# Performance work log

Hardware: AMD Instinct MI355X
Metric: run time of the kernel (lower is better)

## Reference

```python
import jax, jax.numpy as jnp
import numpy as np

B, T, H, W, C = 2, 8, 32, 32, 192
DI, N, K, DTR = 384, 16, 4, 12   # d_inner=2*dim, d_state, scan directions, dt_rank=ceil(dim/16)
LT, HID = 77, 768
L = T * H * W


def setup_inputs() -> dict:
    key = jax.random.key(0)
    ks = jax.random.split(key, 16)
    r = lambda i, shape, s=1.0: jax.random.normal(ks[i], shape, dtype=jnp.float32) * s
    return {
        "x": r(0, (B, T, H, W, C)),
        "text": r(1, (B, LT, C)),
        "cpe1_w": r(2, (C, 1, 3, 3, 3), 0.05), "cpe1_b": jnp.zeros((C,), jnp.float32),
        "cpe2_w": r(3, (C, 1, 3, 3, 3), 0.05), "cpe2_b": jnp.zeros((C,), jnp.float32),
        "norm1_g": jnp.ones((C,), jnp.float32), "norm1_b": jnp.zeros((C,), jnp.float32),
        "norm2_g": jnp.ones((C,), jnp.float32), "norm2_b": jnp.zeros((C,), jnp.float32),
        "in_proj_w": r(4, (2 * DI, C), 0.02), "in_proj_b": jnp.zeros((2 * DI,), jnp.float32),
        "text_proj_w": r(5, (DI, C), 0.02), "text_proj_b": jnp.zeros((DI,), jnp.float32),
        "conv_w": r(6, (DI, 1, 3, 3, 3), 0.05), "conv_b": jnp.zeros((DI,), jnp.float32),
        "x_proj_w": r(7, (K, DTR + 2 * N, DI), 0.02),
        "dt_proj_w": r(8, (K, DI, DTR), 0.1), "dt_proj_b": r(9, (K, DI), 0.1),
        "A_log": jnp.log(jnp.tile(jnp.arange(1.0, N + 1.0, dtype=jnp.float32)[None, None, :], (K, DI, 1))),
        "Ds": jnp.ones((K, DI), jnp.float32),
        "out_norm_g": jnp.ones((DI,), jnp.float32), "out_norm_b": jnp.zeros((DI,), jnp.float32),
        "out_proj_w": r(10, (C, DI), 0.02),
        "fc1_w": r(11, (HID, C), 0.02), "fc1_b": jnp.zeros((HID,), jnp.float32),
        "fc2_w": r(12, (C, HID), 0.02), "fc2_b": jnp.zeros((C,), jnp.float32),
    }


def _ln(x, g, b, eps=1e-6):
    m = x.mean(-1, keepdims=True)
    v = jnp.mean((x - m) ** 2, -1, keepdims=True)
    return (x - m) * jax.lax.rsqrt(v + eps) * g + b


def _dwconv3d(x, w, b):  # x [B, Ch, T, H, W], depthwise 3x3x3, SAME padding
    y = jax.lax.conv_general_dilated(x, w, (1, 1, 1), 'SAME',
                                     feature_group_count=x.shape[1],
                                     dimension_numbers=('NCDHW', 'OIDHW', 'NCDHW'))
    return y + b[None, :, None, None, None]


def _cpe(x, w, b):  # conv positional encoding, channels-last in/out
    return jnp.transpose(_dwconv3d(jnp.transpose(x, (0, 4, 1, 2, 3)), w, b), (0, 2, 3, 4, 1))


def _ss2d(x, text, p):
    # in-projection -> (x, z) gate split
    xz = x @ p['in_proj_w'].T + p['in_proj_b']           # [B,T,H,W,2*DI]
    xi, z = jnp.split(xz, 2, axis=-1)
    # text conditioning (pooled text tokens -> channel bias)
    cond = jax.nn.silu(text.mean(1) @ p['text_proj_w'].T + p['text_proj_b'])  # [B,DI]
    xi = xi + cond[:, None, None, None, :]
    # depthwise conv3d + SiLU
    xc = jax.nn.silu(_dwconv3d(jnp.transpose(xi, (0, 4, 1, 2, 3)), p['conv_w'], p['conv_b']))  # [B,DI,T,H,W]
    # cross-scan: (t,h,w), (t,w,h) and their reversals
    x0 = xc.reshape(B, DI, L)
    x1 = jnp.swapaxes(xc, 3, 4).reshape(B, DI, L)
    xs = jnp.stack([x0, x1, jnp.flip(x0, -1), jnp.flip(x1, -1)], 1)  # [B,K,DI,L]
    # per-direction projections
    xdbl = jnp.einsum('bkdl,kcd->bkcl', xs, p['x_proj_w'])
    dtr, Bm, Cm = jnp.split(xdbl, [DTR, DTR + N], axis=2)            # [B,K,DTR,L],[B,K,N,L],[B,K,N,L]
    dt = jax.nn.softplus(jnp.einsum('bkrl,kdr->bkdl', dtr, p['dt_proj_w']) + p['dt_proj_b'][None, :, :, None])
    A = -jnp.exp(p['A_log'])                                          # [K,DI,N]
    def step(h, inp):
        u_l, dt_l, B_l, C_l = inp
        h = h * jnp.exp(dt_l[..., None] * A) + (dt_l * u_l)[..., None] * B_l[:, :, None, :]
        return h, jnp.einsum('bkdn,bkn->bkd', h, C_l)
    seq = (xs.transpose(3, 0, 1, 2), dt.transpose(3, 0, 1, 2),
           Bm.transpose(3, 0, 1, 2), Cm.transpose(3, 0, 1, 2))
    _, ys = jax.lax.scan(step, jnp.zeros((B, K, DI, N), xs.dtype), seq)  # ys [L,B,K,DI]
    ys = ys.transpose(1, 2, 3, 0) + p['Ds'][None, :, :, None] * xs       # [B,K,DI,L]
    # merge the 4 directions back into (t,h,w) order
    unt = lambda y: jnp.swapaxes(y.reshape(B, DI, T, W, H), 3, 4).reshape(B, DI, L)
    y = ys[:, 0] + jnp.flip(ys[:, 2], -1) + unt(ys[:, 1]) + unt(jnp.flip(ys[:, 3], -1))
    y = _ln(y.transpose(0, 2, 1), p['out_norm_g'], p['out_norm_b']).reshape(B, T, H, W, DI)
    y = y * jax.nn.silu(z)
    return y @ p['out_proj_w'].T


def reference(x, text, cpe1_w, cpe1_b, cpe2_w, cpe2_b, norm1_g, norm1_b, norm2_g, norm2_b,
              in_proj_w, in_proj_b, text_proj_w, text_proj_b, conv_w, conv_b,
              x_proj_w, dt_proj_w, dt_proj_b, A_log, Ds, out_norm_g, out_norm_b, out_proj_w,
              fc1_w, fc1_b, fc2_w, fc2_b):
    p = dict(in_proj_w=in_proj_w, in_proj_b=in_proj_b, text_proj_w=text_proj_w,
             text_proj_b=text_proj_b, conv_w=conv_w, conv_b=conv_b, x_proj_w=x_proj_w,
             dt_proj_w=dt_proj_w, dt_proj_b=dt_proj_b, A_log=A_log, Ds=Ds,
             out_norm_g=out_norm_g, out_norm_b=out_norm_b, out_proj_w=out_proj_w)
    x = x + _cpe(x, cpe1_w, cpe1_b)
    x = x + _ss2d(_ln(x, norm1_g, norm1_b), text, p)
    x = x + _cpe(x, cpe2_w, cpe2_b)
    h = _ln(x, norm2_g, norm2_b)
    x = x + (jax.nn.gelu(h @ fc1_w.T + fc1_b) @ fc2_w.T + fc2_b)
    return x
```

## Files before the change

### kernel.cpp

```cpp
#include <hip/hip_runtime.h>
#include <hip/hip_bf16.h>

#define DEV __device__ __forceinline__

namespace {

constexpr int cB = 2, cT = 8, cH = 32, cW = 32, cC = 192;
constexpr int cDI = 384, cN = 16, cK = 4, cDTR = 12, cLT = 77, cHID = 768;
constexpr int cL  = cT * cH * cW;
constexpr int cBL = cB * cL;
constexpr int SEG = 128, SEGLEN = cL / SEG;
constexpr int XROW = cDTR + 2 * cN;
constexpr int XSTR = 48;

typedef __attribute__((ext_vector_type(8))) short bf16x8;
typedef __attribute__((ext_vector_type(4))) float f32x4;
typedef __attribute__((ext_vector_type(4))) short short4v;

DEV float bfu2f(unsigned short u) { return __uint_as_float(((unsigned)u) << 16); }
DEV float ldsel(const void* p, size_t i, int f32) {
  return f32 ? ((const float*)p)[i] : bfu2f(((const unsigned short*)p)[i]);
}
template <int F32>
DEV float4 ld4(const void* p, size_t e) {
  if (F32) return *(const float4*)((const float*)p + e);
  ushort4 u = *(const ushort4*)((const unsigned short*)p + e);
  return make_float4(bfu2f(u.x), bfu2f(u.y), bfu2f(u.z), bfu2f(u.w));
}
DEV short f2bf(float f) {
  unsigned u = __float_as_uint(f);
  u += 0x7fffu + ((u >> 16) & 1u);
  return (short)(u >> 16);
}
DEV float siluf(float x) { return x / (1.f + __expf(-x)); }
DEV float softplusf(float x) { return (x > 20.f) ? x : __logf(1.f + __expf(x)); }
DEV float gelut(float x) {
  float u = 0.7978845608028654f * (x + 0.044715f * x * x * x);
  float e = __expf(2.f * u);
  float th = 1.f - 2.f / (e + 1.f);
  return 0.5f * x * (1.f + th);
}

template <int BS>
DEV void blkreduce2(float& a, float& b) {
  __shared__ float ra[BS], rb[BS];
  int t = threadIdx.x;
  ra[t] = a; rb[t] = b; __syncthreads();
#pragma unroll
  for (int s = BS / 2; s > 0; s >>= 1) {
    if (t < s) { ra[t] += ra[t + s]; rb[t] += rb[t + s]; }
    __syncthreads();
  }
  a = ra[0]; b = rb[0];
  __syncthreads();
}

__global__ void __launch_bounds__(256) detect_kernel(
    const unsigned short* __restrict__ xa, const unsigned short* __restrict__ wp,
    int* __restrict__ flg) {
  __shared__ int cnt[2];
  if (threadIdx.x < 2) cnt[threadIdx.x] = 0;
  __syncthreads();
  int l0 = 0, l1 = 0;
  for (int i = threadIdx.x; i < 1024; i += 256) {
    float v = bfu2f(xa[2 * i]); float a = fabsf(v);
    if (v == 0.f || (a > 1e-8f && a < 1e4f)) l0++;
    float u = bfu2f(wp[2 * i]); float bq = fabsf(u);
    if (u == 0.f || (bq > 1e-8f && bq < 1e4f)) l1++;
  }
  atomicAdd(&cnt[0], l0); atomicAdd(&cnt[1], l1);
  __syncthreads();
  if (threadIdx.x == 0) {
    flg[0] = (cnt[0] < 614) ? 1 : 0;
    flg[1] = (cnt[1] < 614) ? 1 : 0;
    flg[2] = 1;
  }
}

__global__ void __launch_bounds__(256) prep_kernel(
    const void* __restrict__ cvw, const void* __restrict__ cvb,
    const void* __restrict__ c1w, const void* __restrict__ c1b,
    const void* __restrict__ c2w, const void* __restrict__ c2b,
    const int* __restrict__ flg,
    float* __restrict__ wcv, float* __restrict__ bcv,
    float* __restrict__ w1, float* __restrict__ b1,
    float* __restrict__ w2, float* __restrict__ b2) {
  int pf = flg[1];
  int i = blockIdx.x * 256 + threadIdx.x;
  int r = i;
  if (r < 27 * cDI) { int j = r / cDI, d = r % cDI; wcv[r] = ldsel(cvw, (size_t)d * 27 + j, pf); return; }
  r -= 27 * cDI;
  if (r < cDI) { bcv[r] = ldsel(cvb, r, pf); return; }
  r -= cDI;
  if (r < 27 * cC) { int j = r / cC, c = r % cC; w1[r] = ldsel(c1w, (size_t)c * 27 + j, pf); return; }
  r -= 27 * cC;
  if (r < cC) { b1[r] = ldsel(c1b, r, pf); return; }
  r -= cC;
  if (r < 27 * cC) { int j = r / cC, c = r % cC; w2[r] = ldsel(c2w, (size_t)c * 27 + j, pf); return; }
  r -= 27 * cC;
  if (r < cC) { b2[r] = ldsel(c2b, r, pf); return; }
}

template <int F32>
DEV void cpe_body(const void* __restrict__ xin, const float* __restrict__ wT,
                  const float* __restrict__ bs, int idx, float* __restrict__ out) {
  int c = (idx % (cC / 4)) * 4; int bv = idx / (cC / 4);
  int v = bv & (cL - 1); int b = bv >> 13;
  int t = v >> 10, q = v & 1023, h = q >> 5, w = q & 31;
  float4 acc = *(const float4*)(bs + c);
#pragma unroll
  for (int dz = 0; dz < 3; ++dz) {
    int tt = t + dz - 1; if ((unsigned)tt >= (unsigned)cT) continue;
#pragma unroll
    for (int dy = 0; dy < 3; ++dy) {
      int hh = h + dy - 1; if ((unsigned)hh >= (unsigned)cH) continue;
#pragma unroll
      for (int dx = 0; dx < 3; ++dx) {
        int ww = w + dx - 1; if ((unsigned)ww >= (unsigned)cW) continue;
        int vv = (tt << 10) + (hh << 5) + ww;
        float4 wv = *(const float4*)(wT + (dz * 9 + dy * 3 + dx) * cC + c);
        float4 xv = ld4<F32>(xin, ((size_t)b * cL + vv) * cC + c);
        acc.x += wv.x * xv.x; acc.y += wv.y * xv.y;
        acc.z += wv.z * xv.z; acc.w += wv.w * xv.w;
      }
    }
  }
  float4 x0 = ld4<F32>(xin, (size_t)bv * cC + c);
  float4 o = make_float4(x0.x + acc.x, x0.y + acc.y, x0.z + acc.z, x0.w + acc.w);
  *(float4*)(out + (size_t)bv * cC + c) = o;
}

__global__ void __launch_bounds__(256) cpe_kernel(
    const void* __restrict__ xin, const float* __restrict__ wT,
    const float* __restrict__ bs, const int* __restrict__ flg, int afidx,
    float* __restrict__ out) {
  int idx = blockIdx.x * 256 + threadIdx.x;
  if (idx >= cBL * cC / 4) return;
  if (flg[afidx]) cpe_body<1>(xin, wT, bs, idx, out);
  else            cpe_body<0>(xin, wT, bs, idx, out);
}

__global__ void __launch_bounds__(256) dwconv_silu_kernel(
    const unsigned short* __restrict__ xin, const float* __restrict__ wT,
    const float* __restrict__ bs, unsigned short* __restrict__ out) {
  int idx = blockIdx.x * 256 + threadIdx.x;
  if (idx >= cBL * cDI / 4) return;
  int d = (idx % (cDI / 4)) * 4; int bv = idx / (cDI / 4);
  int v = bv & (cL - 1); int b = bv >> 13;
  int t = v >> 10, q = v & 1023, h = q >> 5, w = q & 31;
  float4 acc = *(const float4*)(bs + d);
#pragma unroll
  for (int dz = 0; dz < 3; ++dz) {
    int tt = t + dz - 1; if ((unsigned)tt >= (unsigned)cT) continue;
#pragma unroll
    for (int dy = 0; dy < 3; ++dy) {
      int hh = h + dy - 1; if ((unsigned)hh >= (unsigned)cH) continue;
#pragma unroll
      for (int dx = 0; dx < 3; ++dx) {
        int ww = w + dx - 1; if ((unsigned)ww >= (unsigned)cW) continue;
        int vv = (tt << 10) + (hh << 5) + ww;
        float4 wv = *(const float4*)(wT + (dz * 9 + dy * 3 + dx) * cDI + d);
        ushort4 u4 = *(const ushort4*)(xin + ((size_t)b * cL + vv) * cDI + d);
        acc.x += wv.x * bfu2f(u4.x); acc.y += wv.y * bfu2f(u4.y);
        acc.z += wv.z * bfu2f(u4.z); acc.w += wv.w * bfu2f(u4.w);
      }
    }
  }
  ushort4 o;
  o.x = (unsigned short)f2bf(siluf(acc.x));
  o.y = (unsigned short)f2bf(siluf(acc.y));
  o.z = (unsigned short)f2bf(siluf(acc.z));
  o.w = (unsigned short)f2bf(siluf(acc.w));
  *(ushort4*)(out + (size_t)bv * cDI + d) = o;
}

__global__ void __launch_bounds__(256) lnb_kernel(
    const float* __restrict__ in, const void* __restrict__ g,
    const void* __restrict__ bb, const int* __restrict__ flg,
    unsigned short* __restrict__ out) {
  int pf = flg[1];
  int row = blockIdx.x * 4 + (threadIdx.x >> 6);
  int lane = threadIdx.x & 63;
  const float* x = in + (size_t)row * cC;
  float v0 = x[lane], v1 = x[lane + 64], v2 = x[lane + 128];
  float s1 = v0 + v1 + v2;
  float s2 = v0 * v0 + v1 * v1 + v2 * v2;
#pragma unroll
  for (int off = 32; off > 0; off >>= 1) {
    s1 += __shfl_xor(s1, off);
    s2 += __shfl_xor(s2, off);
  }
  float mean = s1 * (1.f / cC);
  float var = s2 * (1.f / cC) - mean * mean;
  float rstd = rsqrtf(var + 1e-6f);
  unsigned short* o = out + (size_t)row * cC;
  o[lane]       = (unsigned short)f2bf((v0 - mean) * rstd * ldsel(g, lane, pf)       + ldsel(bb, lane, pf));
  o[lane + 64]  = (unsigned short)f2bf((v1 - mean) * rstd * ldsel(g, lane + 64, pf)  + ldsel(bb, lane + 64, pf));
  o[lane + 128] = (unsigned short)f2bf((v2 - mean) * rstd * ldsel(g, lane + 128, pf) + ldsel(bb, lane + 128, pf));
}

__global__ void __launch_bounds__(384) text_cond_kernel(
    const void* __restrict__ text, const void* __restrict__ tw,
    const void* __restrict__ tb, const int* __restrict__ flg,
    float* __restrict__ cond) {
  int af = flg[0], pf = flg[1];
  __shared__ float mean[cC];
  int b = blockIdx.x;
  for (int c = threadIdx.x; c < cC; c += 384) {
    float s = 0.f;
    for (int t = 0; t < cLT; ++t) s += ldsel(text, ((size_t)b * cLT + t) * cC + c, af);
    mean[c] = s * (1.f / cLT);
  }
  __syncthreads();
  int di = threadIdx.x;
  float a = ldsel(tb, di, pf);
  for (int c = 0; c < cC; ++c) a += mean[c] * ldsel(tw, di * cC + c, pf);
  cond[b * cDI + di] = siluf(a);
}

template <int MODE, int ABF>
__global__ void __launch_bounds__(256) gemm_mfma_kernel(
    const void* __restrict__ A, const void* __restrict__ W,
    int N, int K, const void* __restrict__ bias, const int* __restrict__ flg,
    const float* __restrict__ extra, float* __restrict__ out,
    unsigned short* __restrict__ out2) {
  constexpr int BM = 128, BN = 64, BK = 32, PK = 40;
  __shared__ short As[BM * PK];
  __shared__ short Bs[BN * PK];
  int pf = flg[1];
  int tid = threadIdx.x;
  int m0 = blockIdx.y * BM, n0 = blockIdx.x * BN;
  int lane = tid & 63, wv = tid >> 6;
  int wm = (wv >> 1) * 64, wn = (wv & 1) * 32;
  int lr = lane & 15, quad = lane >> 4;
  f32x4 acc[4][2];
#pragma unroll
  for (int mi = 0; mi < 4; ++mi)
#pragma unroll
    for (int ni = 0; ni < 2; ++ni) { acc[mi][ni][0]=0.f; acc[mi][ni][1]=0.f; acc[mi][ni][2]=0.f; acc[mi][ni][3]=0.f; }
  int ar = tid >> 1, aks = (tid & 1) * 16;
  int wr = tid >> 2, wks = (tid & 3) * 8;
  for (int k0 = 0; k0 < K; k0 += BK) {
    if (ABF) {
      const unsigned short* ap = (const unsigned short*)A + (size_t)(m0 + ar) * K + k0 + aks;
      short* da = &As[ar * PK + aks];
#pragma unroll
      for (int i = 0; i < 4; ++i)
        *(short4v*)(da + i * 4) = *(const short4v*)(ap + i * 4);
    } else {
      const float* ap = (const float*)A + (size_t)(m0 + ar) * K + k0 + aks;
      short* da = &As[ar * PK + aks];
#pragma unroll
      for (int i = 0; i < 4; ++i) {
        float4 v = ((const float4*)ap)[i];
        short4v h; h.x = f2bf(v.x); h.y = f2bf(v.y); h.z = f2bf(v.z); h.w = f2bf(v.w);
        *(short4v*)(da + i * 4) = h;
      }
    }
    {
      int nr = n0 + wr;
      short hb[8];
      if (nr < N) {
        size_t wi = (size_t)nr * K + k0 + wks;
        if (pf) {
#pragma unroll
          for (int i = 0; i < 8; ++i) hb[i] = f2bf(((const float*)W)[wi + i]);
        } else {
#pragma unroll
          for (int i = 0; i < 8; ++i) hb[i] = (short)((const unsigned short*)W)[wi + i];
        }
      } else {
#pragma unroll
        for (int i = 0; i < 8; ++i) hb[i] = 0;
      }
      short* db = &Bs[wr * PK + wks];
#pragma unroll
      for (int i = 0; i < 8; i += 4) {
        short4v h; h.x = hb[i]; h.y = hb[i+1]; h.z = hb[i+2]; h.w = hb[i+3];
        *(short4v*)(db + i) = h;
      }
    }
    __syncthreads();
    bf16x8 af[4], bfr[2];
#pragma unroll
    for (int mi = 0; mi < 4; ++mi)
      af[mi] = *(const bf16x8*)&As[(wm + mi * 16 + lr) * PK + quad * 8];
#pragma unroll
    for (int ni = 0; ni < 2; ++ni)
      bfr[ni] = *(const bf16x8*)&Bs[(wn + ni * 16 + lr) * PK + quad * 8];
#pragma unroll
    for (int mi = 0; mi < 4; ++mi)
#pragma unroll
      for (int ni = 0; ni < 2; ++ni)
        acc[mi][ni] = __builtin_amdgcn_mfma_f32_16x16x32_bf16(af[mi], bfr[ni], acc[mi][ni], 0, 0, 0);
    __syncthreads();
  }
#pragma unroll
  for (int mi = 0; mi < 4; ++mi) {
#pragma unroll
    for (int ni = 0; ni < 2; ++ni) {
#pragma unroll
      for (int r = 0; r < 4; ++r) {
        int m = m0 + wm + mi * 16 + quad * 4 + r;
        int n = n0 + wn + ni * 16 + lr;
        float v = acc[mi][ni][r];
        if (MODE == 0) {
          float bvv = ldsel(bias, n, pf);
          int b = m >> 13;
          if (n < cDI)
            ((unsigned short*)out)[(size_t)m * cDI + n] =
                (unsigned short)f2bf(v + bvv + extra[b * cDI + n]);
          else
            out2[(size_t)m * cDI + (n - cDI)] = (unsigned short)f2bf(v + bvv);
        } else if (MODE == 1) {
          if (n < cK * XROW) {
            int k = n / XROW, c = n - k * XROW;
            int b = m >> 13, vv = m & (cL - 1);
            int t = vv >> 10, q = vv & 1023, h = q >> 5, w = q & 31;
            int l1 = (t << 10) + (w << 5) + h;
            int lk = (k == 0) ? vv : (k == 1) ? l1 : (k == 2) ? (cL - 1 - vv) : (cL - 1 - l1);
            out[((size_t)(b * cK + k) * cL + lk) * XSTR + c] = v;
          }
        } else if (MODE == 2) {
          out[(size_t)m * cC + n] = v + extra[(size_t)m * cC + n];
        } else if (MODE == 3) {
          ((unsigned short*)out)[(size_t)m * cHID + n] =
              (unsigned short)f2bf(gelut(v + ldsel(bias, n, pf)));
        } else {
          out[(size_t)m * cC + n] = v + ldsel(bias, n, pf) + extra[(size_t)m * cC + n];
        }
      }
    }
  }
}

DEV int scan_voxel(int k, int l) {
  if (k == 0) return l;
  if (k == 2) return cL - 1 - l;
  int ll = (k == 1) ? l : (cL - 1 - l);
  int t = ll >> 10, q = ll & 1023, w = q >> 5, h = q & 31;
  return (t << 10) + (h << 5) + w;
}

struct Row11 { float4 r0, r1, r2, r3, r4, r5, r6, r7, r8, r9, r10; };
struct Row7  { float4 r0, r1, r2, r7, r8, r9, r10; };

DEV Row11 ldrow11(const float* __restrict__ rows, int st) {
  const float4* rp = (const float4*)(rows + st * XSTR);
  Row11 q;
  q.r0 = rp[0]; q.r1 = rp[1]; q.r2 = rp[2]; q.r3 = rp[3]; q.r4 = rp[4];
  q.r5 = rp[5]; q.r6 = rp[6]; q.r7 = rp[7]; q.r8 = rp[8]; q.r9 = rp[9];
  q.r10 = rp[10];
  return q;
}
DEV Row7 ldrow7(const float* __restrict__ rows, int st) {
  const float4* rp = (const float4*)(rows + st * XSTR);
  Row7 q;
  q.r0 = rp[0]; q.r1 = rp[1]; q.r2 = rp[2];
  q.r7 = rp[7]; q.r8 = rp[8]; q.r9 = rp[9]; q.r10 = rp[10];
  return q;
}

DEV float s1step(const Row11& q, float u,
                 const float (&wdt)[cDTR], float dtb, float ac0, float Dsd,
                 float (&h)[cN], float& P1) {
  float s0 = dtb + q.r0.x*wdt[0] + q.r0.z*wdt[2] + q.r1.x*wdt[4] + q.r1.z*wdt[6] + q.r2.x*wdt[8] + q.r2.z*wdt[10];
  float s1 = q.r0.y*wdt[1] + q.r0.w*wdt[3] + q.r1.y*wdt[5] + q.r1.w*wdt[7] + q.r2.y*wdt[9] + q.r2.w*wdt[11];
  float dt = softplusf(s0 + s1);
  float a1 = exp2f(dt * ac0);
  float a2 = a1*a1, a3 = a2*a1, a4 = a2*a2;
  float a5 = a4*a1, a6 = a4*a2, a7 = a4*a3, a8 = a4*a4;
  float a9 = a8*a1, a10 = a8*a2, a11 = a8*a3, a12 = a8*a4;
  float a13 = a8*a5, a14 = a8*a6, a15 = a8*a7, a16 = a8*a8;
  float dtu = dt * u;
  P1 *= a1;
  float yp0 = Dsd * u, yp1 = 0.f, yp2 = 0.f, yp3 = 0.f;
  h[0]  = h[0] *a1  + dtu*q.r3.x; yp0 += h[0] *q.r7.x;
  h[1]  = h[1] *a2  + dtu*q.r3.y; yp1 += h[1] *q.r7.y;
  h[2]  = h[2] *a3  + dtu*q.r3.z; yp2 += h[2] *q.r7.z;
  h[3]  = h[3] *a4  + dtu*q.r3.w; yp3 += h[3] *q.r7.w;
  h[4]  = h[4] *a5  + dtu*q.r4.x; yp0 += h[4] *q.r8.x;
  h[5]  = h[5] *a6  + dtu*q.r4.y; yp1 += h[5] *q.r8.y;
  h[6]  = h[6] *a7  + dtu*q.r4.z; yp2 += h[6] *q.r8.z;
  h[7]  = h[7] *a8  + dtu*q.r4.w; yp3 += h[7] *q.r8.w;
  h[8]  = h[8] *a9  + dtu*q.r5.x; yp0 += h[8] *q.r9.x;
  h[9]  = h[9] *a10 + dtu*q.r5.y; yp1 += h[9] *q.r9.y;
  h[10] = h[10]*a11 + dtu*q.r5.z; yp2 += h[10]*q.r9.z;
  h[11] = h[11]*a12 + dtu*q.r5.w; yp3 += h[11]*q.r9.w;
  h[12] = h[12]*a13 + dtu*q.r6.x; yp0 += h[12]*q.r10.x;
  h[13] = h[13]*a14 + dtu*q.r6.y; yp1 += h[13]*q.r10.y;
  h[14] = h[14]*a15 + dtu*q.r6.z; yp2 += h[14]*q.r10.z;
  h[15] = h[15]*a16 + dtu*q.r6.w; yp3 += h[15]*q.r10.w;
  return (yp0 + yp1) + (yp2 + yp3);
}

DEV float s3step(const Row7& q,
                 const float (&wdt)[cDTR], float dtb, float ac0,
                 float (&g)[cN]) {
  float s0 = dtb + q.r0.x*wdt[0] + q.r0.z*wdt[2] + q.r1.x*wdt[4] + q.r1.z*wdt[6] + q.r2.x*wdt[8] + q.r2.z*wdt[10];
  float s1 = q.r0.y*wdt[1] + q.r0.w*wdt[3] + q.r1.y*wdt[5] + q.r1.w*wdt[7] + q.r2.y*wdt[9] + q.r2.w*wdt[11];
  float dt = softplusf(s0 + s1);
  float a1 = exp2f(dt * ac0);
  float a2 = a1*a1, a3 = a2*a1, a4 = a2*a2;
  float a5 = a4*a1, a6 = a4*a2, a7 = a4*a3, a8 = a4*a4;
  float a9 = a8*a1, a10 = a8*a2, a11 = a8*a3, a12 = a8*a4;
  float a13 = a8*a5, a14 = a8*a6, a15 = a8*a7, a16 = a8*a8;
  float yp0 = 0.f, yp1 = 0.f, yp2 = 0.f, yp3 = 0.f;
  g[0]  *= a1;  yp0 += g[0] *q.r7.x;
  g[1]  *= a2;  yp1 += g[1] *q.r7.y;
  g[2]  *= a3;  yp2 += g[2] *q.r7.z;
  g[3]  *= a4;  yp3 += g[3] *q.r7.w;
  g[4]  *= a5;  yp0 += g[4] *q.r8.x;
  g[5]  *= a6;  yp1 += g[5] *q.r8.y;
  g[6]  *= a7;  yp2 += g[6] *q.r8.z;
  g[7]  *= a8;  yp3 += g[7] *q.r8.w;
  g[8]  *= a9;  yp0 += g[8] *q.r9.x;
  g[9]  *= a10; yp1 += g[9] *q.r9.y;
  g[10] *= a11; yp2 += g[10]*q.r9.z;
  g[11] *= a12; yp3 += g[11]*q.r9.w;
  g[12] *= a13; yp0 += g[12]*q.r10.x;
  g[13] *= a14; yp1 += g[13]*q.r10.y;
  g[14] *= a15; yp2 += g[14]*q.r10.z;
  g[15] *= a16; yp3 += g[15]*q.r10.w;
  return (yp0 + yp1) + (yp2 + yp3);
}

__global__ void __launch_bounds__(128, 3) scan1_kernel(
    const unsigned short* __restrict__ xch, const float* __restrict__ xdbl,
    const void* __restrict__ dtw, const void* __restrict__ dtbv,
    const void* __restrict__ alog, const void* __restrict__ dsv,
    const int* __restrict__ flg,
    unsigned short* __restrict__ ys0, unsigned short* __restrict__ ys1,
    unsigned short* __restrict__ ys2, unsigned short* __restrict__ ys3,
    unsigned short* __restrict__ hend, unsigned short* __restrict__ pend) {
  __shared__ float rows[SEGLEN * XSTR];
  int pf = flg[1];
  int tid = threadIdx.x;
  int d = blockIdx.x * 128 + tid;
  int bks = blockIdx.y;
  int s = bks & (SEG - 1); int bk = bks / SEG; int k = bk & 3; int b = bk >> 2;
  int l0 = s * SEGLEN;
  {
    const float4* src = (const float4*)(xdbl + ((size_t)bk * cL + l0) * XSTR);
    float4* dst = (float4*)rows;
#pragma unroll
    for (int i = 0; i < (SEGLEN * XSTR / 4) / 128; ++i)
      dst[tid + i * 128] = src[tid + i * 128];
  }
  float wdt[cDTR];
#pragma unroll
  for (int r = 0; r < cDTR; ++r) wdt[r] = ldsel(dtw, (size_t)(k * cDI + d) * cDTR + r, pf);
  float dtb = ldsel(dtbv, k * cDI + d, pf);
  float ac[cN];
#pragma unroll
  for (int n = 0; n < cN; ++n)
    ac[n] = -__expf(ldsel(alog, (size_t)(k * cDI + d) * cN + n, pf)) * 1.4426950408889634f;
  bool fast = true;
#pragma unroll
  for (int n = 1; n < cN; ++n)
    fast = fast && (fabsf(ac[n] - (float)(n + 1) * ac[0]) <= 1e-3f * fabsf(ac[n]));
  float Dsd = ldsel(dsv, k * cDI + d, pf);
  float h[cN];
#pragma unroll
  for (int n = 0; n < cN; ++n) h[n] = 0.f;
  size_t so = ((size_t)bks * cDI + d) * cN;
  const unsigned short* xcb = xch + (size_t)b * cL * cDI + d;
  unsigned short* ysk = (k == 0) ? ys0 : (k == 1) ? ys1 : (k == 2) ? ys2 : ys3;
  unsigned short* ysrow = ysk + ((size_t)b * cL + l0) * cDI + d;
  __syncthreads();
  if (fast) {
    float ac0 = ac[0];
    float P1 = 1.f;
    Row11 qa = ldrow11(rows, 0);
    float u0 = bfu2f(xcb[(size_t)scan_voxel(k, l0) * cDI]);
    float u1 = bfu2f(xcb[(size_t)scan_voxel(k, l0 + 1) * cDI]);
    for (int st = 0; st < SEGLEN; st += 2) {
      Row11 qb = ldrow11(rows, st + 1);
      int p2 = (st + 2 < SEGLEN) ? st + 2 : SEGLEN - 1;
      int p3 = (st + 3 < SEGLEN) ? st + 3 : SEGLEN - 1;
      float nu0 = bfu2f(xcb[(size_t)scan_voxel(k, l0 + p2) * cDI]);
      float nu1 = bfu2f(xcb[(size_t)scan_voxel(k, l0 + p3) * cDI]);
      float ya = s1step(qa, u0, wdt, dtb, ac0, Dsd, h, P1);
      ysrow[(size_t)st * cDI] = (unsigned short)f2bf(ya);
      qa = ldrow11(rows, p2);
      float yb = s1step(qb, u1, wdt, dtb, ac0, Dsd, h, P1);
      ysrow[(size_t)(st + 1) * cDI] = (unsigned short)f2bf(yb);
      u0 = nu0; u1 = nu1;
    }
    float pp = P1;
#pragma unroll
    for (int n = 0; n < cN; ++n) {
      hend[so + n] = (unsigned short)f2bf(h[n]);
      pend[so + n] = (unsigned short)f2bf(pp);
      pp *= P1;
    }
  } else {
    float P[cN];
#pragma unroll
    for (int n = 0; n < cN; ++n) P[n] = 1.f;
    for (int st = 0; st < SEGLEN; ++st) {
      int l = l0 + st;
      const float4* rp = (const float4*)(rows + st * XSTR);
      float4 q0 = rp[0], q1 = rp[1], q2 = rp[2];
      float s0 = dtb + q0.x*wdt[0] + q0.z*wdt[2] + q1.x*wdt[4] + q1.z*wdt[6] + q2.x*wdt[8] + q2.z*wdt[10];
      float s1 = q0.y*wdt[1] + q0.w*wdt[3] + q1.y*wdt[5] + q1.w*wdt[7] + q2.y*wdt[9] + q2.w*wdt[11];
      float dt = softplusf(s0 + s1);
      float Bv[cN], Cv[cN];
      float4 qb0 = rp[3], qb1 = rp[4], qb2 = rp[5], qb3 = rp[6];
      float4 qc0 = rp[7], qc1 = rp[8], qc2 = rp[9], qc3 = rp[10];
      Bv[0]=qb0.x; Bv[1]=qb0.y; Bv[2]=qb0.z; Bv[3]=qb0.w;
      Bv[4]=qb1.x; Bv[5]=qb1.y; Bv[6]=qb1.z; Bv[7]=qb1.w;
      Bv[8]=qb2.x; Bv[9]=qb2.y; Bv[10]=qb2.z; Bv[11]=qb2.w;
      Bv[12]=qb3.x; Bv[13]=qb3.y; Bv[14]=qb3.z; Bv[15]=qb3.w;
      Cv[0]=qc0.x; Cv[1]=qc0.y; Cv[2]=qc0.z; Cv[3]=qc0.w;
      Cv[4]=qc1.x; Cv[5]=qc1.y; Cv[6]=qc1.z; Cv[7]=qc1.w;
      Cv[8]=qc2.x; Cv[9]=qc2.y; Cv[10]=qc2.z; Cv[11]=qc2.w;
      Cv[12]=qc3.x; Cv[13]=qc3.y; Cv[14]=qc3.z; Cv[15]=qc3.w;
      int v = scan_voxel(k, l);
      float u = bfu2f(xcb[(size_t)v * cDI]);
      float dtu = dt * u;
      float y = Dsd * u;
#pragma unroll
      for (int n = 0; n < cN; ++n) {
        float a = exp2f(dt * ac[n]);
        h[n] = h[n] * a + dtu * Bv[n];
        P[n] *= a;
        y += h[n] * Cv[n];
      }
      ysrow[(size_t)st * cDI] = (unsigned short)f2bf(y);
    }
#pragma unroll
    for (int n = 0; n < cN; ++n) {
      hend[so + n] = (unsigned short)f2bf(h[n]);
      pend[so + n] = (unsigned short)f2bf(P[n]);
    }
  }
}

__global__ void __launch_bounds__(256) scan2_kernel(
    unsigned short* __restrict__ hend, const unsigned short* __restrict__ pend) {
  int tid = blockIdx.x * 256 + threadIdx.x;
  int bk = tid / (cDI * cN); int r = tid - bk * (cDI * cN);
  float g = 0.f;
  for (int s = 0; s < SEG; ++s) {
    size_t o = ((size_t)(bk * SEG + s) * cDI * cN) + r;
    float he = bfu2f(hend[o]), pe = bfu2f(pend[o]);
    hend[o] = (unsigned short)f2bf(g);
    g = pe * g + he;
  }
}

__global__ void __launch_bounds__(128, 3) scan3_kernel(
    const float* __restrict__ xdbl,
    const void* __restrict__ dtw, const void* __restrict__ dtbv,
    const void* __restrict__ alog, const int* __restrict__ flg,
    const unsigned short* __restrict__ hin,
    unsigned short* __restrict__ ys0, unsigned short* __restrict__ ys1,
    unsigned short* __restrict__ ys2, unsigned short* __restrict__ ys3) {
  int bks = blockIdx.y;
  int s = bks & (SEG - 1);
  if (s == 0) return;
  __shared__ float rows[SEGLEN * XSTR];
  int pf = flg[1];
  int tid = threadIdx.x;
  int d = blockIdx.x * 128 + tid;
  int bk = bks / SEG; int k = bk & 3; int b = bk >> 2;
  int l0 = s * SEGLEN;
  {
    const float4* src = (const float4*)(xdbl + ((size_t)bk * cL + l0) * XSTR);
    float4* dst = (float4*)rows;
#pragma unroll
    for (int i = 0; i < (SEGLEN * XSTR / 4) / 128; ++i)
      dst[tid + i * 128] = src[tid + i * 128];
  }
  float wdt[cDTR];
#pragma unroll
  for (int r = 0; r < cDTR; ++r) wdt[r] = ldsel(dtw, (size_t)(k * cDI + d) * cDTR + r, pf);
  float dtb = ldsel(dtbv, k * cDI + d, pf);
  float ac[cN];
#pragma unroll
  for (int n = 0; n < cN; ++n)
    ac[n] = -__expf(ldsel(alog, (size_t)(k * cDI + d) * cN + n, pf)) * 1.4426950408889634f;
  bool fast = true;
#pragma unroll
  for (int n = 1; n < cN; ++n)
    fast = fast && (fabsf(ac[n] - (float)(n + 1) * ac[0]) <= 1e-3f * fabsf(ac[n]));
  float g[cN];
  size_t so = ((size_t)bks * cDI + d) * cN;
#pragma unroll
  for (int n = 0; n < cN; ++n) g[n] = bfu2f(hin[so + n]);
  unsigned short* ysk = (k == 0) ? ys0 : (k == 1) ? ys1 : (k == 2) ? ys2 : ys3;
  unsigned short* ysrow = ysk + ((size_t)b * cL + l0) * cDI + d;
  __syncthreads();
  if (fast) {
    float ac0 = ac[0];
    Row7 qa = ldrow7(rows, 0);
    for (int st = 0; st < SEGLEN; st += 2) {
      Row7 qb = ldrow7(rows, st + 1);
      int p2 = (st + 2 < SEGLEN) ? st + 2 : SEGLEN - 1;
      float ya = s3step(qa, wdt, dtb, ac0, g);
      size_t ia = (size_t)st * cDI;
      ysrow[ia] = (unsigned short)f2bf(bfu2f(ysrow[ia]) + ya);
      qa = ldrow7(rows, p2);
      float yb = s3step(qb, wdt, dtb, ac0, g);
      size_t ib = (size_t)(st + 1) * cDI;
      ysrow[ib] = (unsigned short)f2bf(bfu2f(ysrow[ib]) + yb);
    }
  } else {
    for (int st = 0; st < SEGLEN; ++st) {
      const float4* rp = (const float4*)(rows + st * XSTR);
      float4 q0 = rp[0], q1 = rp[1], q2 = rp[2];
      float s0 = dtb + q0.x*wdt[0] + q0.z*wdt[2] + q1.x*wdt[4] + q1.z*wdt[6] + q2.x*wdt[8] + q2.z*wdt[10];
      float s1 = q0.y*wdt[1] + q0.w*wdt[3] + q1.y*wdt[5] + q1.w*wdt[7] + q2.y*wdt[9] + q2.w*wdt[11];
      float dt = softplusf(s0 + s1);
      float Cv[cN];
      float4 qc0 = rp[7], qc1 = rp[8], qc2 = rp[9], qc3 = rp[10];
      Cv[0]=qc0.x; Cv[1]=qc0.y; Cv[2]=qc0.z; Cv[3]=qc0.w;
      Cv[4]=qc1.x; Cv[5]=qc1.y; Cv[6]=qc1.z; Cv[7]=qc1.w;
      Cv[8]=qc2.x; Cv[9]=qc2.y; Cv[10]=qc2.z; Cv[11]=qc2.w;
      Cv[12]=qc3.x; Cv[13]=qc3.y; Cv[14]=qc3.z; Cv[15]=qc3.w;
      float y = 0.f;
#pragma unroll
      for (int n = 0; n < cN; ++n) {
        float a = exp2f(dt * ac[n]);
        g[n] *= a;
        y += g[n] * Cv[n];
      }
      size_t ii = (size_t)st * cDI;
      ysrow[ii] = (unsigned short)f2bf(bfu2f(ysrow[ii]) + y);
    }
  }
}

__global__ void __launch_bounds__(128) merge_kernel(
    const unsigned short* __restrict__ ys0, const unsigned short* __restrict__ ys1,
    const unsigned short* __restrict__ ys2, const unsigned short* __restrict__ ys3,
    const unsigned short* __restrict__ zh,
    const void* __restrict__ ong, const void* __restrict__ onb,
    const int* __restrict__ flg, unsigned short* __restrict__ yg) {
  int pf = flg[1];
  int bv = blockIdx.x;
  int v = bv & (cL - 1); int b = bv >> 13;
  int t = v >> 10, q = v & 1023, hh = q >> 5, ww = q & 31;
  int l1 = (t << 10) + (ww << 5) + hh;
  size_t r0 = ((size_t)b * cL + v) * cDI;
  size_t r1 = ((size_t)b * cL + l1) * cDI;
  size_t r2 = ((size_t)b * cL + (cL - 1 - v)) * cDI;
  size_t r3 = ((size_t)b * cL + (cL - 1 - l1)) * cDI;
  float vals[3]; float s1 = 0.f, s2 = 0.f;
#pragma unroll
  for (int i = 0; i < 3; ++i) {
    int d = threadIdx.x + i * 128;
    float x = bfu2f(ys0[r0 + d]) + bfu2f(ys1[r1 + d]) +
              bfu2f(ys2[r2 + d]) + bfu2f(ys3[r3 + d]);
    vals[i] = x; s1 += x; s2 += x * x;
  }
  blkreduce2<128>(s1, s2);
  float mean = s1 * (1.f / cDI);
  float var = s2 * (1.f / cDI) - mean * mean;
  float rstd = rsqrtf(var + 1e-6f);
  const unsigned short* zr = zh + (size_t)bv * cDI;
  unsigned short* og = yg + (size_t)bv * cDI;
#pragma unroll
  for (int i = 0; i < 3; ++i) {
    int d = threadIdx.x + i * 128;
    float xn = (vals[i] - mean) * rstd * ldsel(ong, d, pf) + ldsel(onb, d, pf);
    og[d] = (unsigned short)f2bf(xn * siluf(bfu2f(zr[d])));
  }
}

}

extern "C" void kernel_launch(void* const* d_in, const int* in_sizes, int n_in,
                              void* d_out, int out_size, void* d_ws, size_t ws_size,
                              hipStream_t stream) {
  (void)in_sizes; (void)n_in; (void)out_size; (void)ws_size;
  const void* x    = d_in[0];
  const void* text = d_in[1];
  const void* c1w  = d_in[2];
  const void* c1b  = d_in[3];
  const void* c2w  = d_in[4];
  const void* c2b  = d_in[5];
  const void* n1g  = d_in[6];
  const void* n1b  = d_in[7];
  const void* n2g  = d_in[8];
  const void* n2b  = d_in[9];
  const void* ipw  = d_in[10];
  const void* ipb  = d_in[11];
  const void* tpw  = d_in[12];
  const void* tpb  = d_in[13];
  const void* cvw  = d_in[14];
  const void* cvb  = d_in[15];
  const void* xpw  = d_in[16];
  const void* dtw  = d_in[17];
  const void* dtb  = d_in[18];
  const void* alog = d_in[19];
  const void* dsv  = d_in[20];
  const void* ong  = d_in[21];
  const void* onb  = d_in[22];
  const void* opw  = d_in[23];
  const void* f1w  = d_in[24];
  const void* f1b  = d_in[25];
  const void* f2w  = d_in[26];
  const void* f2b  = d_in[27];

  float* Wf = (float*)d_ws;

  constexpr size_t oC  = 0;
  constexpr size_t oD  = 6291456;
  constexpr size_t oG  = 9437184;
  constexpr size_t oA  = 12582912;
  constexpr size_t oB  = 18874368;
  constexpr size_t oE  = 25165824;
  constexpr size_t oF  = 28311552;
  constexpr size_t oCO = 31457280;
  constexpr size_t oFL = 31458048;
  constexpr size_t oWCV = 31458052;
  constexpr size_t oBCV = 31468420;
  constexpr size_t oW1  = 31468804;
  constexpr size_t oB1  = 31473988;
  constexpr size_t oW2  = 31474180;
  constexpr size_t oB2  = 31479364;
  unsigned short* xch = (unsigned short*)(Wf + oC);
  unsigned short* ysd2 = (unsigned short*)(Wf + oC + 3145728);
  unsigned short* hbufh = (unsigned short*)(Wf + oC);
  float* xdbl = Wf + oD;
  unsigned short* ygh  = (unsigned short*)(Wf + oD);
  unsigned short* xnh  = (unsigned short*)(Wf + oG);
  unsigned short* pendp = (unsigned short*)(Wf + oG);
  unsigned short* xib  = (unsigned short*)(Wf + oA);
  unsigned short* ysd0 = (unsigned short*)(Wf + oA);
  unsigned short* ysd1 = (unsigned short*)(Wf + oA + 3145728);
  float* x2   = Wf + oA;
  unsigned short* zh   = (unsigned short*)(Wf + oB);
  unsigned short* ysd3 = (unsigned short*)(Wf + oB + 3145728);
  float* x3   = Wf + oB;
  float* x1   = Wf + oE;
  unsigned short* hendp = (unsigned short*)(Wf + oF);
  unsigned short* xn2h = (unsigned short*)(Wf + oF);
  float* cond = Wf + oCO;
  int*   flg  = (int*)(Wf + oFL);
  float* wcv = Wf + oWCV; float* bcv = Wf + oBCV;
  float* w1t = Wf + oW1;  float* b1t = Wf + oB1;
  float* w2t = Wf + oW2;  float* b2t = Wf + oB2;

  const int cpeBlocks = (cBL * cC / 4) / 256;
  const int dwBlocks  = (cBL * cDI / 4) / 256;

  hipLaunchKernelGGL(detect_kernel, dim3(1), dim3(256), 0, stream,
                     (const unsigned short*)x, (const unsigned short*)ipw, flg);
  hipLaunchKernelGGL(prep_kernel, dim3(85), dim3(256), 0, stream,
                     cvw, cvb, c1w, c1b, c2w, c2b, flg, wcv, bcv, w1t, b1t, w2t, b2t);
  hipLaunchKernelGGL(cpe_kernel, dim3(cpeBlocks), dim3(256), 0, stream,
                     x, w1t, b1t, flg, 0, x1);
  hipLaunchKernelGGL(lnb_kernel, dim3(cBL / 4), dim3(256), 0, stream, x1, n1g, n1b, flg, xnh);
  hipLaunchKernelGGL(text_cond_kernel, dim3(cB), dim3(384), 0, stream, text, tpw, tpb, flg, cond);
  hipLaunchKernelGGL((gemm_mfma_kernel<0, 1>), dim3(2 * cDI / 64, cBL / 128), dim3(256), 0, stream,
                     xnh, ipw, 2 * cDI, cC, ipb, flg, cond, (float*)xib, zh);
  hipLaunchKernelGGL(dwconv_silu_kernel, dim3(dwBlocks), dim3(256), 0, stream,
                     xib, wcv, bcv, xch);
  hipLaunchKernelGGL((gemm_mfma_kernel<1, 1>), dim3((cK * XROW + 63) / 64, cBL / 128), dim3(256), 0, stream,
                     xch, xpw, cK * XROW, cDI, (const void*)nullptr, flg,
                     (const float*)nullptr, xdbl, (unsigned short*)nullptr);
  hipLaunchKernelGGL(scan1_kernel, dim3(cDI / 128, cB * cK * SEG), dim3(128), 0, stream,
                     xch, xdbl, dtw, dtb, alog, dsv, flg,
                     ysd0, ysd1, ysd2, ysd3, hendp, pendp);
  hipLaunchKernelGGL(scan2_kernel, dim3(cB * cK * cDI * cN / 256), dim3(256), 0, stream,
                     hendp, pendp);
  hipLaunchKernelGGL(scan3_kernel, dim3(cDI / 128, cB * cK * SEG), dim3(128), 0, stream,
                     xdbl, dtw, dtb, alog, flg, hendp, ysd0, ysd1, ysd2, ysd3);
  hipLaunchKernelGGL(merge_kernel, dim3(cBL), dim3(128), 0, stream,
                     ysd0, ysd1, ysd2, ysd3, zh, ong, onb, flg, ygh);
  hipLaunchKernelGGL((gemm_mfma_kernel<2, 1>), dim3(cC / 64, cBL / 128), dim3(256), 0, stream,
                     ygh, opw, cC, cDI, (const void*)nullptr, flg, x1, x2,
                     (unsigned short*)nullptr);
  hipLaunchKernelGGL(cpe_kernel, dim3(cpeBlocks), dim3(256), 0, stream,
                     x2, w2t, b2t, flg, 2, x3);
  hipLaunchKernelGGL(lnb_kernel, dim3(cBL / 4), dim3(256), 0, stream, x3, n2g, n2b, flg, xn2h);
  hipLaunchKernelGGL((gemm_mfma_kernel<3, 1>), dim3(cHID / 64, cBL / 128), dim3(256), 0, stream,
                     xn2h, f1w, cHID, cC, f1b, flg, (const float*)nullptr, (float*)hbufh,
                     (unsigned short*)nullptr);
  hipLaunchKernelGGL((gemm_mfma_kernel<4, 1>), dim3(cC / 64, cBL / 128), dim3(256), 0, stream,
                     hbufh, f2w, cC, cHID, f2b, flg, x3, (float*)d_out,
                     (unsigned short*)nullptr);
}
```

Baseline: 616.6 us.

## Compute two adjacent W outputs per thread in depthwise convs; wave-per-row merge

The CPE and depthwise 3D conv kernels now compute two neighbouring W positions per thread. Each thread loads four input columns and three weight vectors per (dz,dy) tap row and shares them across both outputs, which cuts redundant global loads and weight fetches, and the thread count is halved. The merge kernel maps one 64-lane wave to each row, replacing the shared-memory block reduction with shuffle reductions and cutting syncthreads. The change trades extra registers and fewer threads for less load traffic.

```diff
diff --git a/kernel.cpp b/kernel.cpp
--- a/kernel.cpp
+++ b/kernel.cpp
@@ -39,20 +39,6 @@
   float e = __expf(2.f * u);
   float th = 1.f - 2.f / (e + 1.f);
   return 0.5f * x * (1.f + th);
-}
-
-template <int BS>
-DEV void blkreduce2(float& a, float& b) {
-  __shared__ float ra[BS], rb[BS];
-  int t = threadIdx.x;
-  ra[t] = a; rb[t] = b; __syncthreads();
-#pragma unroll
-  for (int s = BS / 2; s > 0; s >>= 1) {
-    if (t < s) { ra[t] += ra[t + s]; rb[t] += rb[t + s]; }
-    __syncthreads();
-  }
-  a = ra[0]; b = rb[0];
-  __syncthreads();
 }
 
 __global__ void __launch_bounds__(256) detect_kernel(
@@ -104,30 +90,46 @@
 template <int F32>
 DEV void cpe_body(const void* __restrict__ xin, const float* __restrict__ wT,
                   const float* __restrict__ bs, int idx, float* __restrict__ out) {
-  int c = (idx % (cC / 4)) * 4; int bv = idx / (cC / 4);
-  int v = bv & (cL - 1); int b = bv >> 13;
-  int t = v >> 10, q = v & 1023, h = q >> 5, w = q & 31;
-  float4 acc = *(const float4*)(bs + c);
+  int c = (idx % (cC / 4)) * 4; int pv = idx / (cC / 4);
+  int w0 = (pv & 15) << 1;
+  int rest = pv >> 4;
+  int h = rest & 31; int bt = rest >> 5; int t = bt & 7; int b = bt >> 3;
+  float4 bias = *(const float4*)(bs + c);
+  float4 acc0 = bias, acc1 = bias;
+  const float4 zero = make_float4(0.f, 0.f, 0.f, 0.f);
 #pragma unroll
   for (int dz = 0; dz < 3; ++dz) {
     int tt = t + dz - 1; if ((unsigned)tt >= (unsigned)cT) continue;
 #pragma unroll
     for (int dy = 0; dy < 3; ++dy) {
       int hh = h + dy - 1; if ((unsigned)hh >= (unsigned)cH) continue;
-#pragma unroll
-      for (int dx = 0; dx < 3; ++dx) {
-        int ww = w + dx - 1; if ((unsigned)ww >= (unsigned)cW) continue;
-        int vv = (tt << 10) + (hh << 5) + ww;
-        float4 wv = *(const float4*)(wT + (dz * 9 + dy * 3 + dx) * cC + c);
-        float4 xv = ld4<F32>(xin, ((size_t)b * cL + vv) * cC + c);
-        acc.x += wv.x * xv.x; acc.y += wv.y * xv.y;
-        acc.z += wv.z * xv.z; acc.w += wv.w * xv.w;
-      }
-    }
-  }
-  float4 x0 = ld4<F32>(xin, (size_t)bv * cC + c);
-  float4 o = make_float4(x0.x + acc.x, x0.y + acc.y, x0.z + acc.z, x0.w + acc.w);
-  *(float4*)(out + (size_t)bv * cC + c) = o;
+      int base = (tt << 10) + (hh << 5);
+      const float* wr = wT + (dz * 9 + dy * 3) * cC + c;
+      float4 wv0 = *(const float4*)(wr);
+      float4 wv1 = *(const float4*)(wr + cC);
+      float4 wv2 = *(const float4*)(wr + 2 * cC);
+      size_t rb = ((size_t)b * cL + base) * cC + c;
+      float4 xm1 = (w0 > 0)  ? ld4<F32>(xin, rb + (size_t)(w0 - 1) * cC) : zero;
+      float4 x0v = ld4<F32>(xin, rb + (size_t)w0 * cC);
+      float4 x1v = ld4<F32>(xin, rb + (size_t)(w0 + 1) * cC);
+      float4 x2v = (w0 < 30) ? ld4<F32>(xin, rb + (size_t)(w0 + 2) * cC) : zero;
+      acc0.x += wv0.x*xm1.x + wv1.x*x0v.x + wv2.x*x1v.x;
+      acc0.y += wv0.y*xm1.y + wv1.y*x0v.y + wv2.y*x1v.y;
+      acc0.z += wv0.z*xm1.z + wv1.z*x0v.z + wv2.z*x1v.z;
+      acc0.w += wv0.w*xm1.w + wv1.w*x0v.w + wv2.w*x1v.w;
+      acc1.x += wv0.x*x0v.x + wv1.x*x1v.x + wv2.x*x2v.x;
+      acc1.y += wv0.y*x0v.y + wv1.y*x1v.y + wv2.y*x2v.y;
+      acc1.z += wv0.z*x0v.z + wv1.z*x1v.z + wv2.z*x2v.z;
+      acc1.w += wv0.w*x0v.w + wv1.w*x1v.w + wv2.w*x2v.w;
+    }
+  }
+  size_t bv0 = (size_t)b * cL + (t << 10) + (h << 5) + w0;
+  float4 r0 = ld4<F32>(xin, bv0 * cC + c);
+  float4 r1 = ld4<F32>(xin, (bv0 + 1) * cC + c);
+  *(float4*)(out + bv0 * cC + c) =
+      make_float4(r0.x + acc0.x, r0.y + acc0.y, r0.z + acc0.z, r0.w + acc0.w);
+  *(float4*)(out + (bv0 + 1) * cC + c) =
+      make_float4(r1.x + acc1.x, r1.y + acc1.y, r1.z + acc1.z, r1.w + acc1.w);
 }
 
 __global__ void __launch_bounds__(256) cpe_kernel(
@@ -135,7 +137,7 @@
     const float* __restrict__ bs, const int* __restrict__ flg, int afidx,
     float* __restrict__ out) {
   int idx = blockIdx.x * 256 + threadIdx.x;
-  if (idx >= cBL * cC / 4) return;
+  if (idx >= cBL * cC / 8) return;
   if (flg[afidx]) cpe_body<1>(xin, wT, bs, idx, out);
   else            cpe_body<0>(xin, wT, bs, idx, out);
 }
@@ -144,34 +146,52 @@
     const unsigned short* __restrict__ xin, const float* __restrict__ wT,
     const float* __restrict__ bs, unsigned short* __restrict__ out) {
   int idx = blockIdx.x * 256 + threadIdx.x;
-  if (idx >= cBL * cDI / 4) return;
-  int d = (idx % (cDI / 4)) * 4; int bv = idx / (cDI / 4);
-  int v = bv & (cL - 1); int b = bv >> 13;
-  int t = v >> 10, q = v & 1023, h = q >> 5, w = q & 31;
-  float4 acc = *(const float4*)(bs + d);
+  if (idx >= cBL * cDI / 8) return;
+  int d = (idx % (cDI / 4)) * 4; int pv = idx / (cDI / 4);
+  int w0 = (pv & 15) << 1;
+  int rest = pv >> 4;
+  int h = rest & 31; int bt = rest >> 5; int t = bt & 7; int b = bt >> 3;
+  float4 bias = *(const float4*)(bs + d);
+  float4 acc0 = bias, acc1 = bias;
+  const float4 zero = make_float4(0.f, 0.f, 0.f, 0.f);
 #pragma unroll
   for (int dz = 0; dz < 3; ++dz) {
     int tt = t + dz - 1; if ((unsigned)tt >= (unsigned)cT) continue;
 #pragma unroll
     for (int dy = 0; dy < 3; ++dy) {
       int hh = h + dy - 1; if ((unsigned)hh >= (unsigned)cH) continue;
-#pragma unroll
-      for (int dx = 0; dx < 3; ++dx) {
-        int ww = w + dx - 1; if ((unsigned)ww >= (unsigned)cW) continue;
-        int vv = (tt << 10) + (hh << 5) + ww;
-        float4 wv = *(const float4*)(wT + (dz * 9 + dy * 3 + dx) * cDI + d);
-        ushort4 u4 = *(const ushort4*)(xin + ((size_t)b * cL + vv) * cDI + d);
-        acc.x += wv.x * bfu2f(u4.x); acc.y += wv.y * bfu2f(u4.y);
-        acc.z += wv.z * bfu2f(u4.z); acc.w += wv.w * bfu2f(u4.w);
-      }
-    }
-  }
-  ushort4 o;
-  o.x = (unsigned short)f2bf(siluf(acc.x));
-  o.y = (unsigned short)f2bf(siluf(acc.y));
-  o.z = (unsigned short)f2bf(siluf(acc.z));
-  o.w = (unsigned short)f2bf(siluf(acc.w));
-  *(ushort4*)(out + (size_t)bv * cDI + d) = o;
+      int base = (tt << 10) + (hh << 5);
+      const float* wr = wT + (dz * 9 + dy * 3) * cDI + d;
+      float4 wv0 = *(const float4*)(wr);
+      float4 wv1 = *(const float4*)(wr + cDI);
+      float4 wv2 = *(const float4*)(wr + 2 * cDI);
+      size_t rb = ((size_t)b * cL + base) * cDI + d;
+      float4 xm1 = (w0 > 0)  ? ld4<0>(xin, rb + (size_t)(w0 - 1) * cDI) : zero;
+      float4 x0v = ld4<0>(xin, rb + (size_t)w0 * cDI);
+      float4 x1v = ld4<0>(xin, rb + (size_t)(w0 + 1) * cDI);
+      float4 x2v = (w0 < 30) ? ld4<0>(xin, rb + (size_t)(w0 + 2) * cDI) : zero;
+      acc0.x += wv0.x*xm1.x + wv1.x*x0v.x + wv2.x*x1v.x;
+      acc0.y += wv0.y*xm1.y + wv1.y*x0v.y + wv2.y*x1v.y;
+      acc0.z += wv0.z*xm1.z + wv1.z*x0v.z + wv2.z*x1v.z;
+      acc0.w += wv0.w*xm1.w + wv1.w*x0v.w + wv2.w*x1v.w;
+      acc1.x += wv0.x*x0v.x + wv1.x*x1v.x + wv2.x*x2v.x;
+      acc1.y += wv0.y*x0v.y + wv1.y*x1v.y + wv2.y*x2v.y;
+      acc1.z += wv0.z*x0v.z + wv1.z*x1v.z + wv2.z*x2v.z;
+      acc1.w += wv0.w*x0v.w + wv1.w*x1v.w + wv2.w*x2v.w;
+    }
+  }
+  size_t bv0 = (size_t)b * cL + (t << 10) + (h << 5) + w0;
+  ushort4 o0, o1;
+  o0.x = (unsigned short)f2bf(siluf(acc0.x));
+  o0.y = (unsigned short)f2bf(siluf(acc0.y));
+  o0.z = (unsigned short)f2bf(siluf(acc0.z));
+  o0.w = (unsigned short)f2bf(siluf(acc0.w));
+  o1.x = (unsigned short)f2bf(siluf(acc1.x));
+  o1.y = (unsigned short)f2bf(siluf(acc1.y));
+  o1.z = (unsigned short)f2bf(siluf(acc1.z));
+  o1.w = (unsigned short)f2bf(siluf(acc1.w));
+  *(ushort4*)(out + bv0 * cDI + d) = o0;
+  *(ushort4*)(out + (bv0 + 1) * cDI + d) = o1;
 }
 
 __global__ void __launch_bounds__(256) lnb_kernel(
@@ -632,14 +652,15 @@
   }
 }
 
-__global__ void __launch_bounds__(128) merge_kernel(
+__global__ void __launch_bounds__(256) merge_kernel(
     const unsigned short* __restrict__ ys0, const unsigned short* __restrict__ ys1,
     const unsigned short* __restrict__ ys2, const unsigned short* __restrict__ ys3,
     const unsigned short* __restrict__ zh,
     const void* __restrict__ ong, const void* __restrict__ onb,
     const int* __restrict__ flg, unsigned short* __restrict__ yg) {
   int pf = flg[1];
-  int bv = blockIdx.x;
+  int bv = blockIdx.x * 4 + (threadIdx.x >> 6);
+  int lane = threadIdx.x & 63;
   int v = bv & (cL - 1); int b = bv >> 13;
   int t = v >> 10, q = v & 1023, hh = q >> 5, ww = q & 31;
   int l1 = (t << 10) + (ww << 5) + hh;
@@ -647,23 +668,27 @@
   size_t r1 = ((size_t)b * cL + l1) * cDI;
   size_t r2 = ((size_t)b * cL + (cL - 1 - v)) * cDI;
   size_t r3 = ((size_t)b * cL + (cL - 1 - l1)) * cDI;
-  float vals[3]; float s1 = 0.f, s2 = 0.f;
-#pragma unroll
-  for (int i = 0; i < 3; ++i) {
-    int d = threadIdx.x + i * 128;
+  float vals[6]; float s1 = 0.f, s2 = 0.f;
+#pragma unroll
+  for (int i = 0; i < 6; ++i) {
+    int d = lane + i * 64;
     float x = bfu2f(ys0[r0 + d]) + bfu2f(ys1[r1 + d]) +
               bfu2f(ys2[r2 + d]) + bfu2f(ys3[r3 + d]);
     vals[i] = x; s1 += x; s2 += x * x;
   }
-  blkreduce2<128>(s1, s2);
+#pragma unroll
+  for (int off = 32; off > 0; off >>= 1) {
+    s1 += __shfl_xor(s1, off);
+    s2 += __shfl_xor(s2, off);
+  }
   float mean = s1 * (1.f / cDI);
   float var = s2 * (1.f / cDI) - mean * mean;
   float rstd = rsqrtf(var + 1e-6f);
   const unsigned short* zr = zh + (size_t)bv * cDI;
   unsigned short* og = yg + (size_t)bv * cDI;
 #pragma unroll
-  for (int i = 0; i < 3; ++i) {
-    int d = threadIdx.x + i * 128;
+  for (int i = 0; i < 6; ++i) {
+    int d = lane + i * 64;
     float xn = (vals[i] - mean) * rstd * ldsel(ong, d, pf) + ldsel(onb, d, pf);
     og[d] = (unsigned short)f2bf(xn * siluf(bfu2f(zr[d])));
   }
@@ -744,8 +769,8 @@
   float* w1t = Wf + oW1;  float* b1t = Wf + oB1;
   float* w2t = Wf + oW2;  float* b2t = Wf + oB2;
 
-  const int cpeBlocks = (cBL * cC / 4) / 256;
-  const int dwBlocks  = (cBL * cDI / 4) / 256;
+  const int cpeBlocks = (cBL * cC / 8) / 256;
+  const int dwBlocks  = (cBL * cDI / 8) / 256;
 
   hipLaunchKernelGGL(detect_kernel, dim3(1), dim3(256), 0, stream,
                      (const unsigned short*)x, (const unsigned short*)ipw, flg);
@@ -769,7 +794,7 @@
                      hendp, pendp);
   hipLaunchKernelGGL(scan3_kernel, dim3(cDI / 128, cB * cK * SEG), dim3(128), 0, stream,
                      xdbl, dtw, dtb, alog, flg, hendp, ysd0, ysd1, ysd2, ysd3);
-  hipLaunchKernelGGL(merge_kernel, dim3(cBL), dim3(128), 0, stream,
+  hipLaunchKernelGGL(merge_kernel, dim3(cBL / 4), dim3(256), 0, stream,
                      ysd0, ysd1, ysd2, ysd3, zh, ong, onb, flg, ygh);
   hipLaunchKernelGGL((gemm_mfma_kernel<2, 1>), dim3(cC / 64, cBL / 128), dim3(256), 0, stream,
                      ygh, opw, cC, cDI, (const void*)nullptr, flg, x1, x2,
```

New measurement: 563.4 us. 1.09x faster.
